# Performance work log

Measured on AMD Instinct MI355X. Metric: run time of the kernel, lower is better.

The kernel has to match this reference:

```python
import jax, jax.numpy as jnp
import numpy as np

N_SKILL = 50000
B = 4096          # number of (job, resume) pairs; n_job == n_resume required by the concat
E = 65536         # edges per relation (avg degree 16)
D = 1536          # embedding_dim
HID = [512, 256, 64]


def setup_inputs() -> dict:
    key = jax.random.key(0)
    ks = jax.random.split(key, 16)
    nrm = lambda k, shape, s=0.02: jax.random.normal(k, shape, dtype=jnp.float32) * s
    inp = {
        "x_skill": jax.random.normal(ks[0], (N_SKILL, D), dtype=jnp.float32),
        "x_job": jax.random.normal(ks[1], (B, D), dtype=jnp.float32),
        "x_resume": jax.random.normal(ks[2], (B, D), dtype=jnp.float32),
        "src_sj": jax.random.randint(ks[3], (E,), 0, N_SKILL),
        "dst_sj": jax.random.randint(ks[4], (E,), 0, B),
        "src_sr": jax.random.randint(ks[5], (E,), 0, N_SKILL),
        "dst_sr": jax.random.randint(ks[6], (E,), 0, B),
        "W_rel_j": nrm(ks[7], (D, D)),
        "b_rel_j": jnp.zeros((D,), jnp.float32),
        "W_root_j": nrm(ks[8], (D, D)),
        "W_rel_r": nrm(ks[9], (D, D)),
        "b_rel_r": jnp.zeros((D,), jnp.float32),
        "W_root_r": nrm(ks[10], (D, D)),
        "W1": nrm(ks[11], (2 * D, HID[0])), "b1": jnp.zeros((HID[0],), jnp.float32),
        "W2": nrm(ks[12], (HID[0], HID[1])), "b2": jnp.zeros((HID[1],), jnp.float32),
        "W3": nrm(ks[13], (HID[1], HID[2])), "b3": jnp.zeros((HID[2],), jnp.float32),
        "W4": nrm(ks[14], (HID[2], 1)), "b4": jnp.zeros((1,), jnp.float32),
    }
    return inp


def _graph_conv(x_src, x_dst, src, dst, W_rel, b_rel, W_root):
    # PyG GraphConv (aggr='add', bipartite): out = lin_rel(sum_{j in N(i)} x_j) + lin_root(x_i)
    agg = jax.ops.segment_sum(x_src[src], dst, num_segments=x_dst.shape[0])  # [B, D]
    return agg @ W_rel + b_rel + x_dst @ W_root


def reference(x_skill, x_job, x_resume, src_sj, dst_sj, src_sr, dst_sr,
              W_rel_j, b_rel_j, W_root_j, W_rel_r, b_rel_r, W_root_r,
              W1, b1, W2, b2, W3, b3, W4, b4):
    # HeteroConv: each dst node type ('job', 'resume') receives exactly one relation,
    # so the cross-relation 'mean' aggregation is the identity.
    h_job = jax.nn.relu(_graph_conv(x_skill, x_job, src_sj, dst_sj, W_rel_j, b_rel_j, W_root_j))
    h_res = jax.nn.relu(_graph_conv(x_skill, x_resume, src_sr, dst_sr, W_rel_r, b_rel_r, W_root_r))
    h = jnp.concatenate([h_job, h_res], axis=1)  # [B, 2D]
    # MLP (dropout is inference-mode identity)
    h = jax.nn.relu(h @ W1 + b1)
    h = jax.nn.relu(h @ W2 + b2)
    h = jax.nn.relu(h @ W3 + b3)
    score = (h @ W4 + b4).squeeze(-1)  # [B]
    return score
```

## Files before the change

### kernel.cpp

```cpp
#include <hip/hip_runtime.h>

#define E_EDGES 65536
#define NB 4096
#define DD 1536
#define CAP 96

typedef unsigned short u16;
typedef __bf16 bf16x8 __attribute__((ext_vector_type(8)));
typedef float f32x4 __attribute__((ext_vector_type(4)));

#define AS1(p) ((const __attribute__((address_space(1))) void*)(p))
#define AS3(p) ((__attribute__((address_space(3))) void*)(p))

#define BAR() do { __builtin_amdgcn_s_barrier(); asm volatile("" ::: "memory"); } while (0)
#define VMCNT0() asm volatile("s_waitcnt vmcnt(0)" ::: "memory")

__device__ __forceinline__ u16 f2bf(float f) {
    unsigned u = __float_as_uint(f);
    u += 0x7fffu + ((u >> 16) & 1u);
    return (u16)(u >> 16);
}


__global__ __launch_bounds__(256) void prep_kernel(
    const float* __restrict__ w0, const float* __restrict__ w1,
    const float* __restrict__ w2, const float* __restrict__ w3,
    const float* __restrict__ w4, const float* __restrict__ w5,
    u16* __restrict__ Wjt, u16* __restrict__ Wrt,
    u16* __restrict__ W1t, u16* __restrict__ W2t,
    const int* __restrict__ sj, const int* __restrict__ dj,
    const int* __restrict__ sr, const int* __restrict__ dr,
    int* __restrict__ cnt, int* __restrict__ bkt) {
    int bid = blockIdx.x;
    if (bid >= 10880) {
        int b2 = bid - 10880;
        int rel = b2 >> 8;
        int e = (b2 & 255) * 256 + threadIdx.x;
        int s = rel ? sr[e] : sj[e];
        int d = rel ? dr[e] : dj[e];
        int slot = rel * NB + d;
        int pos = atomicAdd(&cnt[slot], 1);
        if (pos < CAP) bkt[(size_t)slot * CAP + pos] = s;
        return;
    }
    const float* in; u16* out; int N, ldo, k0, nbx;
    if (bid < 9216) {
        int m = bid / 2304;
        bid = bid % 2304;
        in = (m == 0) ? w0 : (m == 1) ? w1 : (m == 2) ? w2 : w3;
        out = (m < 2) ? Wjt : Wrt;
        N = 1536; ldo = 3072; k0 = (m & 1) ? DD : 0; nbx = 48;
    } else if (bid < 10752) {
        bid -= 9216;
        in = w4; out = W1t; N = 512; ldo = 3072; k0 = 0; nbx = 16;
    } else {
        bid -= 10752;
        in = w5; out = W2t; N = 256; ldo = 512; k0 = 0; nbx = 8;
    }
    int bx = (bid % nbx) * 32;
    int by = (bid / nbx) * 32;
    __shared__ float tile[32][33];
    int tx = threadIdx.x & 31, ty = threadIdx.x >> 5;
#pragma unroll
    for (int i = 0; i < 4; ++i)
        tile[ty + i * 8][tx] = in[(size_t)(by + ty + i * 8) * N + bx + tx];
    __syncthreads();
#pragma unroll
    for (int i = 0; i < 4; ++i) {
        int n = bx + ty + i * 8;
        int k = by + tx;
        out[(size_t)n * ldo + k0 + k] = f2bf(tile[tx][ty + i * 8]);
    }
}


__global__ __launch_bounds__(128) void agg_cvt_kernel(
    const float* __restrict__ xskill, const float* __restrict__ xj, const float* __restrict__ xr,
    const int* __restrict__ bkt, const int* __restrict__ cnt,
    u16* __restrict__ Aj, u16* __restrict__ Ar) {
    int rel = blockIdx.y;
    int row = blockIdx.x;
    int t = threadIdx.x;
    const float* xd = (rel ? xr : xj) + (size_t)row * DD;
    u16* A = (rel ? Ar : Aj) + (size_t)row * (2 * DD);

    float4 v[3];
#pragma unroll
    for (int c = 0; c < 3; ++c) v[c] = *(const float4*)(xd + t * 4 + c * 512);
#pragma unroll
    for (int c = 0; c < 3; ++c) {
        ushort4 o = {f2bf(v[c].x), f2bf(v[c].y), f2bf(v[c].z), f2bf(v[c].w)};
        *(ushort4*)(A + DD + t * 4 + c * 512) = o;
    }

    int count = cnt[rel * NB + row];
    if (count > CAP) count = CAP;
    __shared__ int sidx[CAP];
    if (t < count) sidx[t] = bkt[(size_t)(rel * NB + row) * CAP + t];
    __syncthreads();

    float4 acc[3] = {};
    for (int e = 0; e < count; ++e) {
        const float* xs = xskill + (size_t)sidx[e] * DD;
#pragma unroll
        for (int c = 0; c < 3; ++c) {
            float4 u = *(const float4*)(xs + t * 4 + c * 512);
            acc[c].x += u.x; acc[c].y += u.y; acc[c].z += u.z; acc[c].w += u.w;
        }
    }
#pragma unroll
    for (int c = 0; c < 3; ++c) {
        ushort4 o = {f2bf(acc[c].x), f2bf(acc[c].y), f2bf(acc[c].z), f2bf(acc[c].w)};
        *(ushort4*)(A + t * 4 + c * 512) = o;
    }
}


__global__ __launch_bounds__(512, 2) void conv_gemm(
    const u16* __restrict__ Aj, const u16* __restrict__ Wjt, const float* __restrict__ bj,
    const u16* __restrict__ Ar, const u16* __restrict__ Wrt, const float* __restrict__ br,
    u16* __restrict__ C) {
    constexpr int K = 3072, NT = K / 64, LDC = 3072;
    constexpr int BUF = 28672;
    __shared__ u16 lds[2 * BUF];
    int tid = threadIdx.x;
    int lane = tid & 63;
    int w = tid >> 6;

    int p = blockIdx.y * 16 + blockIdx.x;
    int lg = (p & 7) * 16 + (p >> 3);
    long bm = (long)(lg & 15) * 256;
    long bn = (long)(lg >> 4) * 192;

    const u16* A; const u16* Bt; const float* bias; long cofs;
    if (blockIdx.z) { A = Ar; Bt = Wrt; bias = br; cofs = DD; }
    else            { A = Aj; Bt = Wjt; bias = bj; cofs = 0;  }

    int wm = (w >> 2) * 128;
    int wn = (w & 3) * 48;

    const int srow = lane >> 3;
    const int skf = ((lane & 7) * 8) ^ ((lane >> 3) << 3);

    auto stageA = [&](int b, long k0) {
#pragma unroll
        for (int i = 0; i < 4; ++i) {
            int g = i * 8 + w;
            const u16* gp = A + (bm + g * 8 + srow) * (long)K + k0 + skf;
            __builtin_amdgcn_global_load_lds(AS1(gp), AS3(lds + b * BUF + g * 512), 16, 0, 0);
        }
    };
    auto stageB = [&](int b, long k0) {
#pragma unroll
        for (int i = 0; i < 3; ++i) {
            int g = i * 8 + w;
            const u16* gp = Bt + (bn + g * 8 + srow) * (long)K + k0 + skf;
            __builtin_amdgcn_global_load_lds(AS1(gp), AS3(lds + b * BUF + 16384 + g * 512), 16, 0, 0);
        }
    };

    const int lrow = lane & 15;
    const int lko = (lane >> 4) * 8;
    const int rsw = (lane & 7) << 3;

    auto ldA = [&](int b, int mi, int kk) -> bf16x8 {
        return *(const bf16x8*)(lds + b * BUF + (wm + mi * 16 + lrow) * 64 + ((kk + lko) ^ rsw));
    };
    auto ldB = [&](int b, int nj, int kk) -> bf16x8 {
        return *(const bf16x8*)(lds + b * BUF + 16384 + (wn + nj * 16 + lrow) * 64 + ((kk + lko) ^ rsw));
    };

    f32x4 acc[8][3] = {};

    stageA(0, 0); stageB(0, 0);

    for (int t = 0; t < NT; ++t) {
        int b = t & 1;
        VMCNT0();
        BAR();
        if (t + 1 < NT) {
            long k1 = (long)(t + 1) * 64;
            stageA(b ^ 1, k1); stageB(b ^ 1, k1);
        }
#pragma unroll
        for (int kk = 0; kk < 64; kk += 32) {
            bf16x8 bfr[3];
#pragma unroll
            for (int nj = 0; nj < 3; ++nj) bfr[nj] = ldB(b, nj, kk);
#pragma unroll
            for (int h = 0; h < 2; ++h) {
                bf16x8 af[4];
#pragma unroll
                for (int mi = 0; mi < 4; ++mi) af[mi] = ldA(b, h * 4 + mi, kk);
                __builtin_amdgcn_s_setprio(1);
#pragma unroll
                for (int mi = 0; mi < 4; ++mi)
#pragma unroll
                    for (int nj = 0; nj < 3; ++nj)
                        acc[h * 4 + mi][nj] = __builtin_amdgcn_mfma_f32_16x16x32_bf16(af[mi], bfr[nj], acc[h * 4 + mi][nj], 0, 0, 0);
                __builtin_amdgcn_s_setprio(0);
            }
        }
    }

    int rb = (lane >> 4) * 4, cl = lane & 15;
#pragma unroll
    for (int mi = 0; mi < 8; ++mi)
#pragma unroll
        for (int nj = 0; nj < 3; ++nj) {
            long row = bm + wm + mi * 16 + rb;
            long col = bn + wn + nj * 16 + cl;
            float bb = bias[col];
#pragma unroll
            for (int r = 0; r < 4; ++r) {
                float v = fmaxf(acc[mi][nj][r] + bb, 0.f);
                C[(row + r) * (long)LDC + cofs + col] = f2bf(v);
            }
        }
}


template <int BM, bool OUT_BF16>
__global__ __launch_bounds__(256) void gemm_bias_relu(
    const u16* __restrict__ A, const u16* __restrict__ Bt, const float* __restrict__ bias,
    void* __restrict__ C, int K, int ldc) {
    constexpr int BK = 64;
    constexpr int MI = BM / 32;
    constexpr int NITER = (BM + 128) / 32;
    __shared__ u16 lA[BM * BK];
    __shared__ u16 lB[128 * BK];
    int tid = threadIdx.x;
    int lane = tid & 63;
    int w = tid >> 6;
    long bm = (long)blockIdx.x * BM;
    long bn = (long)blockIdx.y * 128;
    int wm = (w >> 1) * (BM / 2), wn = (w & 1) * 64;
    f32x4 acc[MI][4] = {};
    const int lrow = lane & 15;
    const int lko = (lane >> 4) * 8;

    for (int k0 = 0; k0 < K; k0 += BK) {
#pragma unroll
        for (int i = 0; i < NITER; ++i) {
            int chunk = i * 256 + tid;
            int row = chunk >> 3, kc = chunk & 7;
            if (row < BM) {
                const u16* g = A + (bm + row) * (long)K + k0 + kc * 8;
                __builtin_amdgcn_global_load_lds(AS1(g), AS3((char*)lA + i * 4096 + w * 1024), 16, 0, 0);
            } else {
                const u16* g = Bt + (bn + row - BM) * (long)K + k0 + kc * 8;
                __builtin_amdgcn_global_load_lds(AS1(g), AS3((char*)lB + i * 4096 + w * 1024 - BM * 128), 16, 0, 0);
            }
        }
        __syncthreads();
#pragma unroll
        for (int kk = 0; kk < BK; kk += 32) {
            bf16x8 af[MI], bfr[4];
#pragma unroll
            for (int i = 0; i < MI; ++i)
                af[i] = *(const bf16x8*)(lA + (wm + i * 16 + lrow) * BK + kk + lko);
#pragma unroll
            for (int j = 0; j < 4; ++j)
                bfr[j] = *(const bf16x8*)(lB + (wn + j * 16 + lrow) * BK + kk + lko);
#pragma unroll
            for (int i = 0; i < MI; ++i)
#pragma unroll
                for (int j = 0; j < 4; ++j)
                    acc[i][j] = __builtin_amdgcn_mfma_f32_16x16x32_bf16(af[i], bfr[j], acc[i][j], 0, 0, 0);
        }
        __syncthreads();
    }

    int rb = (lane >> 4) * 4, cl = lane & 15;
#pragma unroll
    for (int i = 0; i < MI; ++i)
#pragma unroll
        for (int j = 0; j < 4; ++j) {
            long row = bm + wm + i * 16 + rb;
            long col = bn + wn + j * 16 + cl;
            float b = bias[col];
#pragma unroll
            for (int r = 0; r < 4; ++r) {
                float v = fmaxf(acc[i][j][r] + b, 0.f);
                long o = (row + r) * (long)ldc + col;
                if (OUT_BF16)
                    ((u16*)C)[o] = f2bf(v);
                else
                    ((float*)C)[o] = v;
            }
        }
}


__global__ __launch_bounds__(256) void l34_kernel(
    const float* __restrict__ h2, const float* __restrict__ W3, const float* __restrict__ b3,
    const float* __restrict__ W4, const float* __restrict__ b4, float* __restrict__ out) {
    __shared__ float W3s[256 * 64];
    __shared__ float hbuf[4][256];
    int tid = threadIdx.x;
#pragma unroll
    for (int i = 0; i < 16; ++i)
        ((float4*)W3s)[tid + i * 256] = ((const float4*)W3)[tid + i * 256];
    __syncthreads();
    int w = tid >> 6, t = tid & 63;
    float w4t = W4[t];
    float b3t = b3[t];
    float b40 = b4[0];
    for (int rr = 0; rr < 4; ++rr) {
        int row = blockIdx.x * 16 + w * 4 + rr;
        ((float4*)hbuf[w])[t] = ((const float4*)(h2 + (size_t)row * 256))[t];
        float acc = b3t;
#pragma unroll 8
        for (int k = 0; k < 256; ++k) acc = fmaf(hbuf[w][k], W3s[k * 64 + t], acc);
        acc = fmaxf(acc, 0.f);
        float s = acc * w4t;
#pragma unroll
        for (int o = 32; o > 0; o >>= 1) s += __shfl_down(s, o);
        if (t == 0) out[row] = s + b40;
    }
}


extern "C" void kernel_launch(void* const* d_in, const int* in_sizes, int n_in,
                              void* d_out, int out_size, void* d_ws, size_t ws_size,
                              hipStream_t stream) {
    (void)in_sizes; (void)n_in; (void)out_size; (void)ws_size;
    const float* x_skill  = (const float*)d_in[0];
    const float* x_job    = (const float*)d_in[1];
    const float* x_resume = (const float*)d_in[2];
    const int* src_sj = (const int*)d_in[3];
    const int* dst_sj = (const int*)d_in[4];
    const int* src_sr = (const int*)d_in[5];
    const int* dst_sr = (const int*)d_in[6];
    const float* W_rel_j  = (const float*)d_in[7];
    const float* b_rel_j  = (const float*)d_in[8];
    const float* W_root_j = (const float*)d_in[9];
    const float* W_rel_r  = (const float*)d_in[10];
    const float* b_rel_r  = (const float*)d_in[11];
    const float* W_root_r = (const float*)d_in[12];
    const float* W1 = (const float*)d_in[13];
    const float* b1 = (const float*)d_in[14];
    const float* W2 = (const float*)d_in[15];
    const float* b2 = (const float*)d_in[16];
    const float* W3 = (const float*)d_in[17];
    const float* b3 = (const float*)d_in[18];
    const float* W4 = (const float*)d_in[19];
    const float* b4 = (const float*)d_in[20];
    float* out = (float*)d_out;

    char* p = (char*)d_ws;
    auto alloc = [&](size_t bytes) -> char* {
        char* r = p;
        p += (bytes + 255) & ~(size_t)255;
        return r;
    };
    int* cnt = (int*)alloc(2 * NB * 4);
    int* bkt = (int*)alloc((size_t)2 * NB * CAP * 4);
    u16* Aj   = (u16*)alloc((size_t)NB * 2 * DD * 2);
    u16* Ar   = (u16*)alloc((size_t)NB * 2 * DD * 2);
    u16* Wjt  = (u16*)alloc((size_t)DD * 2 * DD * 2);
    u16* Wrt  = (u16*)alloc((size_t)DD * 2 * DD * 2);
    u16* W1t  = (u16*)alloc((size_t)512 * 3072 * 2);
    u16* W2t  = (u16*)alloc((size_t)256 * 512 * 2);
    u16* hcat = (u16*)alloc((size_t)NB * 3072 * 2);
    u16* h1   = (u16*)alloc((size_t)NB * 512 * 2);
    float* h2 = (float*)alloc((size_t)NB * 256 * 4);

    hipMemsetAsync(cnt, 0, 2 * NB * 4, stream);
    prep_kernel<<<11392, 256, 0, stream>>>(W_rel_j, W_root_j, W_rel_r, W_root_r, W1, W2,
                                           Wjt, Wrt, W1t, W2t,
                                           src_sj, dst_sj, src_sr, dst_sr, cnt, bkt);
    agg_cvt_kernel<<<dim3(NB, 2), 128, 0, stream>>>(x_skill, x_job, x_resume, bkt, cnt, Aj, Ar);

    conv_gemm<<<dim3(16, 8, 2), 512, 0, stream>>>(Aj, Wjt, b_rel_j, Ar, Wrt, b_rel_r, hcat);
    gemm_bias_relu<64, true><<<dim3(NB / 64, 512 / 128), 256, 0, stream>>>(hcat, W1t, b1, h1, 3072, 512);
    gemm_bias_relu<64, false><<<dim3(NB / 64, 256 / 128), 256, 0, stream>>>(h1, W2t, b2, h2, 512, 256);
    l34_kernel<<<NB / 16, 256, 0, stream>>>(h2, W3, b3, W4, b4, out);
}
```

Baseline: 329.0 us.

## Split skill aggregation into two source-half passes for cache locality

Edges are bucketed by whether the source skill index falls in the lower or upper half of the skill table. Aggregation then runs as two passes, each touching only half of x_skill (about 150MB), so the gathered rows have a better chance of staying in the last-level cache. The cost is an extra fp32 partial-sum buffer that is written and read back, plus one more kernel launch. The per-bucket cap also drops to 48, which could truncate a high-degree half-bucket.

New measurement: 346.5 us. 5.3% more time.

```diff
diff --git a/kernel.cpp b/kernel.cpp
--- a/kernel.cpp
+++ b/kernel.cpp
@@ -3,7 +3,8 @@
 #define E_EDGES 65536
 #define NB 4096
 #define DD 1536
-#define CAP 96
+#define CAP 48
+#define HALF_SRC 25000
 
 typedef unsigned short u16;
 typedef __bf16 bf16x8 __attribute__((ext_vector_type(8)));
@@ -38,7 +39,8 @@
         int e = (b2 & 255) * 256 + threadIdx.x;
         int s = rel ? sr[e] : sj[e];
         int d = rel ? dr[e] : dj[e];
-        int slot = rel * NB + d;
+        int half = (s >= HALF_SRC) ? 1 : 0;
+        int slot = ((rel << 1) | half) * NB + d;
         int pos = atomicAdd(&cnt[slot], 1);
         if (pos < CAP) bkt[(size_t)slot * CAP + pos] = s;
         return;
@@ -74,32 +76,45 @@
 }
 
 
-__global__ __launch_bounds__(128) void agg_cvt_kernel(
+template <int PASS>
+__global__ __launch_bounds__(128) void agg_pass_kernel(
     const float* __restrict__ xskill, const float* __restrict__ xj, const float* __restrict__ xr,
     const int* __restrict__ bkt, const int* __restrict__ cnt,
-    u16* __restrict__ Aj, u16* __restrict__ Ar) {
+    float* __restrict__ P, u16* __restrict__ Aj, u16* __restrict__ Ar) {
     int rel = blockIdx.y;
     int row = blockIdx.x;
     int t = threadIdx.x;
-    const float* xd = (rel ? xr : xj) + (size_t)row * DD;
+    int slot = ((rel << 1) | PASS) * NB + row;
     u16* A = (rel ? Ar : Aj) + (size_t)row * (2 * DD);
-
-    float4 v[3];
-#pragma unroll
-    for (int c = 0; c < 3; ++c) v[c] = *(const float4*)(xd + t * 4 + c * 512);
-#pragma unroll
-    for (int c = 0; c < 3; ++c) {
-        ushort4 o = {f2bf(v[c].x), f2bf(v[c].y), f2bf(v[c].z), f2bf(v[c].w)};
-        *(ushort4*)(A + DD + t * 4 + c * 512) = o;
-    }
-
-    int count = cnt[rel * NB + row];
+    float* Pr = P + ((size_t)rel * NB + row) * DD;
+
+    if (PASS == 0) {
+        const float* xd = (rel ? xr : xj) + (size_t)row * DD;
+        float4 v[3];
+#pragma unroll
+        for (int c = 0; c < 3; ++c) v[c] = *(const float4*)(xd + t * 4 + c * 512);
+#pragma unroll
+        for (int c = 0; c < 3; ++c) {
+            ushort4 o = {f2bf(v[c].x), f2bf(v[c].y), f2bf(v[c].z), f2bf(v[c].w)};
+            *(ushort4*)(A + DD + t * 4 + c * 512) = o;
+        }
+    }
+
+    int count = cnt[slot];
     if (count > CAP) count = CAP;
     __shared__ int sidx[CAP];
-    if (t < count) sidx[t] = bkt[(size_t)(rel * NB + row) * CAP + t];
+    if (t < count) sidx[t] = bkt[(size_t)slot * CAP + t];
     __syncthreads();
 
-    float4 acc[3] = {};
+    float4 acc[3];
+    if (PASS == 0) {
+#pragma unroll
+        for (int c = 0; c < 3; ++c) acc[c] = float4{0.f, 0.f, 0.f, 0.f};
+    } else {
+#pragma unroll
+        for (int c = 0; c < 3; ++c) acc[c] = *(const float4*)(Pr + t * 4 + c * 512);
+    }
+
     for (int e = 0; e < count; ++e) {
         const float* xs = xskill + (size_t)sidx[e] * DD;
 #pragma unroll
@@ -108,10 +123,16 @@
             acc[c].x += u.x; acc[c].y += u.y; acc[c].z += u.z; acc[c].w += u.w;
         }
     }
-#pragma unroll
-    for (int c = 0; c < 3; ++c) {
-        ushort4 o = {f2bf(acc[c].x), f2bf(acc[c].y), f2bf(acc[c].z), f2bf(acc[c].w)};
-        *(ushort4*)(A + t * 4 + c * 512) = o;
+
+    if (PASS == 0) {
+#pragma unroll
+        for (int c = 0; c < 3; ++c) *(float4*)(Pr + t * 4 + c * 512) = acc[c];
+    } else {
+#pragma unroll
+        for (int c = 0; c < 3; ++c) {
+            ushort4 o = {f2bf(acc[c].x), f2bf(acc[c].y), f2bf(acc[c].z), f2bf(acc[c].w)};
+            *(ushort4*)(A + t * 4 + c * 512) = o;
+        }
     }
 }
 
@@ -354,8 +375,9 @@
         p += (bytes + 255) & ~(size_t)255;
         return r;
     };
-    int* cnt = (int*)alloc(2 * NB * 4);
-    int* bkt = (int*)alloc((size_t)2 * NB * CAP * 4);
+    int* cnt = (int*)alloc(4 * NB * 4);
+    int* bkt = (int*)alloc((size_t)4 * NB * CAP * 4);
+    float* P  = (float*)alloc((size_t)2 * NB * DD * 4);
     u16* Aj   = (u16*)alloc((size_t)NB * 2 * DD * 2);
     u16* Ar   = (u16*)alloc((size_t)NB * 2 * DD * 2);
     u16* Wjt  = (u16*)alloc((size_t)DD * 2 * DD * 2);
@@ -366,11 +388,12 @@
     u16* h1   = (u16*)alloc((size_t)NB * 512 * 2);
     float* h2 = (float*)alloc((size_t)NB * 256 * 4);
 
-    hipMemsetAsync(cnt, 0, 2 * NB * 4, stream);
+    hipMemsetAsync(cnt, 0, 4 * NB * 4, stream);
     prep_kernel<<<11392, 256, 0, stream>>>(W_rel_j, W_root_j, W_rel_r, W_root_r, W1, W2,
                                            Wjt, Wrt, W1t, W2t,
                                            src_sj, dst_sj, src_sr, dst_sr, cnt, bkt);
-    agg_cvt_kernel<<<dim3(NB, 2), 128, 0, stream>>>(x_skill, x_job, x_resume, bkt, cnt, Aj, Ar);
+    agg_pass_kernel<0><<<dim3(NB, 2), 128, 0, stream>>>(x_skill, x_job, x_resume, bkt, cnt, P, Aj, Ar);
+    agg_pass_kernel<1><<<dim3(NB, 2), 128, 0, stream>>>(x_skill, x_job, x_resume, bkt, cnt, P, Aj, Ar);
 
     conv_gemm<<<dim3(16, 8, 2), 512, 0, stream>>>(Aj, Wjt, b_rel_j, Ar, Wrt, b_rel_r, hcat);
     gemm_bias_relu<64, true><<<dim3(NB / 64, 512 / 128), 256, 0, stream>>>(hcat, W1t, b1, h1, 3072, 512);
```
